# Optimization experiments

Measured on AMD Instinct MI355X. Metric: run time of the kernel, lower is better.

Reference implementation:

```python
import jax, jax.numpy as jnp
import numpy as np

D_EV, D_RGB, D_FUSED, D_REASON = 128, 128, 384, 384
D_INNER, D_STATE, D_CONV, DT_RANK = 2 * D_REASON, 16, 4, (D_REASON + 15) // 16
B, L = 4, 1024
LN_EPS = 1e-5


def setup_inputs() -> dict:
    key = jax.random.key(0)
    ks = jax.random.split(key, 16)
    s = lambda k, shp, scale=0.02: jax.random.normal(k, shp, jnp.float32) * scale
    inp = {
        "ev_tok": jax.random.normal(ks[0], (B, L, D_EV), jnp.float32),
        "rgb_tok": jax.random.normal(ks[1], (B, L, D_RGB), jnp.float32),
        "W_ev": s(ks[2], (D_EV, D_FUSED // 2)), "b_ev": jnp.zeros((D_FUSED // 2,), jnp.float32),
        "W_rgb": s(ks[3], (D_RGB, D_FUSED // 2)), "b_rgb": jnp.zeros((D_FUSED // 2,), jnp.float32),
        "ln_g": jnp.ones((D_FUSED,), jnp.float32), "ln_b": jnp.zeros((D_FUSED,), jnp.float32),
        "W_proj": s(ks[4], (D_FUSED, D_REASON)), "b_proj": jnp.zeros((D_REASON,), jnp.float32),
        "W_in": s(ks[5], (D_REASON, 2 * D_INNER)),
        "conv_w": s(ks[6], (D_INNER, 1, D_CONV), 0.1), "conv_b": jnp.zeros((D_INNER,), jnp.float32),
        "W_x": s(ks[7], (D_INNER, DT_RANK + 2 * D_STATE)),
        "W_dt": s(ks[8], (DT_RANK, D_INNER), 0.1), "b_dt": s(ks[9], (D_INNER,), 0.1),
        "A_log": jnp.tile(jnp.log(jnp.arange(1, D_STATE + 1, dtype=jnp.float32)), (D_INNER, 1)),
        "D_skip": jnp.ones((D_INNER,), jnp.float32),
        "W_out": s(ks[10], (D_INNER, D_REASON)),
    }
    return inp


def _selective_scan(u, delta, A, Bm, Cm, D_skip):
    # u, delta: [B,L,d]; Bm, Cm: [B,L,n]; A: [d,n]; D_skip: [d]
    deltaA = jnp.exp(delta[..., None] * A)                       # [B,L,d,n]
    deltaBu = delta[..., None] * Bm[:, :, None, :] * u[..., None]  # [B,L,d,n]

    def step(h, inp):
        dA, dBu, C_t = inp
        h = dA * h + dBu                                         # [B,d,n]
        y = jnp.einsum('bdn,bn->bd', h, C_t)
        return h, y

    h0 = jnp.zeros((u.shape[0], A.shape[0], A.shape[1]), u.dtype)
    xs = (jnp.moveaxis(deltaA, 1, 0), jnp.moveaxis(deltaBu, 1, 0), jnp.moveaxis(Cm, 1, 0))
    _, ys = jax.lax.scan(step, h0, xs)                           # [L,B,d]
    return jnp.moveaxis(ys, 0, 1) + u * D_skip


def _mamba_block(x, W_in, conv_w, conv_b, W_x, W_dt, b_dt, A_log, D_skip, W_out):
    xr = x @ W_in                                                # [B,L,2*d_inner]
    u, res = jnp.split(xr, 2, axis=-1)
    # causal depthwise conv over time
    uc = jnp.swapaxes(u, 1, 2)                                   # [B,d_inner,L]
    uc = jax.lax.conv_general_dilated(uc, conv_w, (1,), [(D_CONV - 1, 0)],
                                      dimension_numbers=('NCH', 'OIH', 'NCH'),
                                      feature_group_count=D_INNER)
    u = jax.nn.silu(jnp.swapaxes(uc, 1, 2) + conv_b)             # [B,L,d_inner]
    x_dbl = u @ W_x                                              # [B,L,dt_rank+2n]
    dt, Bm, Cm = jnp.split(x_dbl, [DT_RANK, DT_RANK + D_STATE], axis=-1)
    delta = jax.nn.softplus(dt @ W_dt + b_dt)                    # [B,L,d_inner]
    A = -jnp.exp(A_log)                                          # [d_inner,n]
    y = _selective_scan(u, delta, A, Bm, Cm, D_skip)
    y = y * jax.nn.silu(res)
    return y @ W_out


def reference(ev_tok, rgb_tok, W_ev, b_ev, W_rgb, b_rgb, ln_g, ln_b, W_proj, b_proj,
              W_in, conv_w, conv_b, W_x, W_dt, b_dt, A_log, D_skip, W_out):
    x = jnp.concatenate([ev_tok @ W_ev + b_ev, rgb_tok @ W_rgb + b_rgb], axis=-1)
    mu = jnp.mean(x, axis=-1, keepdims=True)
    var = jnp.mean(jnp.square(x - mu), axis=-1, keepdims=True)
    x = (x - mu) * jax.lax.rsqrt(var + LN_EPS) * ln_g + ln_b
    x = x @ W_proj + b_proj                                      # [B,L,d_reason]
    return _mamba_block(x, W_in, conv_w, conv_b, W_x, W_dt, b_dt, A_log, D_skip, W_out)
```

## Files before the change

kernel.cpp:

```cpp
#include <hip/hip_runtime.h>
#include <cstddef>
#include <cstdint>

#define L_SEQ 1024
#define NCHUNK 64
#define CLEN 16

typedef __bf16 bf16x8 __attribute__((ext_vector_type(8)));
typedef float f32x4 __attribute__((ext_vector_type(4)));

__device__ __forceinline__ float silu_f(float x) {
    return x / (1.f + __expf(-x));
}

__device__ __forceinline__ float exp2_fast(float x) {
    return exp2f(x);
}

__device__ __forceinline__ unsigned short f2bf(float x) {
    union { float f; unsigned int u; } v; v.f = x;
    unsigned int r = (v.u + 0x7fffu + ((v.u >> 16) & 1u)) >> 16;
    return (unsigned short)r;
}
__device__ __forceinline__ float bf2f(unsigned short h) {
    union { float f; unsigned int u; } v; v.u = ((unsigned int)h) << 16;
    return v.f;
}
__device__ __forceinline__ unsigned int packf(float x) {
    unsigned short h = f2bf(x);
    unsigned short l = f2bf(x - bf2f(h));
    return ((unsigned int)h << 16) | (unsigned int)l;
}
__device__ __forceinline__ float unpackf(unsigned int pk) {
    return bf2f((unsigned short)(pk >> 16)) + bf2f((unsigned short)(pk & 0xffffu));
}

template<bool APK, int EPI>
__global__ __launch_bounds__(256)
void gemm_bf3(const unsigned short* __restrict__ Ahi,
              const unsigned short* __restrict__ Alo,
              const unsigned int* __restrict__ Apk, int lda,
              const unsigned short* __restrict__ Bthi,
              const unsigned short* __restrict__ Btlo,
              const float* __restrict__ bias,
              float* __restrict__ Cf, float* __restrict__ Cf2,
              unsigned short* __restrict__ Chi, unsigned short* __restrict__ Clo,
              int ldc, int K)
{
    __shared__ unsigned short As[2][2][128][40];
    __shared__ unsigned short Bs[2][2][128][40];
    const int tid = threadIdx.x;
    const int lane = tid & 63;
    const int wave = tid >> 6;
    const int wm = wave >> 1, wn = wave & 1;

    const int gx = gridDim.x;
    const int nwg = gx * gridDim.y;
    const int lin = blockIdx.y * gx + blockIdx.x;
    const int chunk = nwg >> 3;
    const int swz = (lin & 7) * chunk + (lin >> 3);
    const int m0 = (swz / gx) * 128, n0 = (swz % gx) * 128;

    const int srow = tid >> 1, sko = (tid & 1) * 16;

    f32x4 acc[4][4];
    #pragma unroll
    for (int i = 0; i < 4; ++i)
        #pragma unroll
        for (int j = 0; j < 4; ++j) {
            f32x4 z = {0.f, 0.f, 0.f, 0.f};
            acc[i][j] = z;
        }

    const size_t aoff = (size_t)(m0 + srow) * lda + sko;
    const size_t boff = (size_t)(n0 + srow) * K + sko;

    uint4 ra[4], rb[4];

    auto load_regs = [&](int k0) {
        if constexpr (APK) {
            const unsigned int* ap = Apk + aoff + k0;
            ra[0] = *(const uint4*)(ap);
            ra[1] = *(const uint4*)(ap + 4);
            ra[2] = *(const uint4*)(ap + 8);
            ra[3] = *(const uint4*)(ap + 12);
        } else {
            ra[0] = *(const uint4*)(Ahi + aoff + k0);
            ra[1] = *(const uint4*)(Ahi + aoff + k0 + 8);
            ra[2] = *(const uint4*)(Alo + aoff + k0);
            ra[3] = *(const uint4*)(Alo + aoff + k0 + 8);
        }
        rb[0] = *(const uint4*)(Bthi + boff + k0);
        rb[1] = *(const uint4*)(Bthi + boff + k0 + 8);
        rb[2] = *(const uint4*)(Btlo + boff + k0);
        rb[3] = *(const uint4*)(Btlo + boff + k0 + 8);
    };

    auto store_lds = [&](int buf) {
        uint4 h0, h1, l0, l1;
        if constexpr (APK) {
            uint4 p0 = ra[0], p1 = ra[1], p2 = ra[2], p3 = ra[3];
            h0.x = (p0.x >> 16) | (p0.y & 0xffff0000u);
            h0.y = (p0.z >> 16) | (p0.w & 0xffff0000u);
            h0.z = (p1.x >> 16) | (p1.y & 0xffff0000u);
            h0.w = (p1.z >> 16) | (p1.w & 0xffff0000u);
            h1.x = (p2.x >> 16) | (p2.y & 0xffff0000u);
            h1.y = (p2.z >> 16) | (p2.w & 0xffff0000u);
            h1.z = (p3.x >> 16) | (p3.y & 0xffff0000u);
            h1.w = (p3.z >> 16) | (p3.w & 0xffff0000u);
            l0.x = (p0.x & 0xffffu) | (p0.y << 16);
            l0.y = (p0.z & 0xffffu) | (p0.w << 16);
            l0.z = (p1.x & 0xffffu) | (p1.y << 16);
            l0.w = (p1.z & 0xffffu) | (p1.w << 16);
            l1.x = (p2.x & 0xffffu) | (p2.y << 16);
            l1.y = (p2.z & 0xffffu) | (p2.w << 16);
            l1.z = (p3.x & 0xffffu) | (p3.y << 16);
            l1.w = (p3.z & 0xffffu) | (p3.w << 16);
        } else {
            h0 = ra[0]; h1 = ra[1]; l0 = ra[2]; l1 = ra[3];
        }
        *(uint4*)&As[buf][0][srow][sko]     = h0;
        *(uint4*)&As[buf][0][srow][sko + 8] = h1;
        *(uint4*)&As[buf][1][srow][sko]     = l0;
        *(uint4*)&As[buf][1][srow][sko + 8] = l1;
        *(uint4*)&Bs[buf][0][srow][sko]     = rb[0];
        *(uint4*)&Bs[buf][0][srow][sko + 8] = rb[1];
        *(uint4*)&Bs[buf][1][srow][sko]     = rb[2];
        *(uint4*)&Bs[buf][1][srow][sko + 8] = rb[3];
    };

    const int fr = lane & 15, kq = lane >> 4;

    load_regs(0);
    store_lds(0);
    __syncthreads();

    int cur = 0;
    for (int k0 = 32; ; k0 += 32) {
        const bool more = k0 < K;
        if (more) load_regs(k0);
        {
            bf16x8 aH[4], aL[4];
            #pragma unroll
            for (int i = 0; i < 4; ++i) {
                aH[i] = *(const bf16x8*)&As[cur][0][wm * 64 + i * 16 + fr][kq * 8];
                aL[i] = *(const bf16x8*)&As[cur][1][wm * 64 + i * 16 + fr][kq * 8];
            }
            #pragma unroll
            for (int j = 0; j < 4; ++j) {
                bf16x8 bH = *(const bf16x8*)&Bs[cur][0][wn * 64 + j * 16 + fr][kq * 8];
                bf16x8 bL = *(const bf16x8*)&Bs[cur][1][wn * 64 + j * 16 + fr][kq * 8];
                #pragma unroll
                for (int i = 0; i < 4; ++i)
                    acc[i][j] = __builtin_amdgcn_mfma_f32_16x16x32_bf16(aH[i], bH, acc[i][j], 0, 0, 0);
                #pragma unroll
                for (int i = 0; i < 4; ++i)
                    acc[i][j] = __builtin_amdgcn_mfma_f32_16x16x32_bf16(aL[i], bH, acc[i][j], 0, 0, 0);
                #pragma unroll
                for (int i = 0; i < 4; ++i)
                    acc[i][j] = __builtin_amdgcn_mfma_f32_16x16x32_bf16(aH[i], bL, acc[i][j], 0, 0, 0);
            }
        }
        if (!more) break;
        store_lds(cur ^ 1);
        __syncthreads();
        cur ^= 1;
    }

    const int col = lane & 15, rq = lane >> 4;
    #pragma unroll
    for (int j = 0; j < 4; ++j) {
        int nn = n0 + wn * 64 + j * 16 + col;
        float bv = 0.f;
        if constexpr (EPI == 0 || EPI == 1) { if (bias) bv = bias[nn]; }
        if constexpr (EPI == 2) { if (nn >= 32 && nn < 800) bv = bias[nn - 32]; }
        #pragma unroll
        for (int i = 0; i < 4; ++i) {
            int mb = m0 + wm * 64 + i * 16 + rq * 4;
            #pragma unroll
            for (int r = 0; r < 4; ++r) {
                float o = acc[i][j][r] + bv;
                if constexpr (EPI == 0) {
                    Cf[(size_t)(mb + r) * ldc + nn] = o;
                } else if constexpr (EPI == 1) {
                    unsigned short h = f2bf(o);
                    Chi[(size_t)(mb + r) * ldc + nn] = h;
                    Clo[(size_t)(mb + r) * ldc + nn] = f2bf(o - bf2f(h));
                } else {
                    if (nn < 32) {
                        Cf2[(size_t)(mb + r) * 32 + nn] = o;
                    } else if (nn < 800) {
                        float sp = fmaxf(o, 0.f) + log1pf(expf(-fabsf(o)));
                        Cf[(size_t)(mb + r) * ldc + (nn - 32)] = sp;
                    }
                }
            }
        }
    }
}

__device__ __forceinline__ void wcvt_body(const float* __restrict__ W,
                                          unsigned short* __restrict__ Thi,
                                          unsigned short* __restrict__ Tlo,
                                          int K, int N, int nx, int local, int tid,
                                          float* t )
{
    const int n0 = (local % nx) * 32, k0 = (local / nx) * 32;
    const int r = tid >> 3, c4 = (tid & 7) * 4;
    float4 v = *(const float4*)(W + (size_t)(k0 + r) * N + n0 + c4);
    t[r * 33 + c4 + 0] = v.x; t[r * 33 + c4 + 1] = v.y;
    t[r * 33 + c4 + 2] = v.z; t[r * 33 + c4 + 3] = v.w;
    __syncthreads();
    unsigned short hs[4], ls[4];
    #pragma unroll
    for (int j = 0; j < 4; ++j) {
        float x = t[(c4 + j) * 33 + r];
        hs[j] = f2bf(x);
        ls[j] = f2bf(x - bf2f(hs[j]));
    }
    size_t o = (size_t)(n0 + r) * K + k0 + c4;
    uint2 hv, lv;
    hv.x = (unsigned)hs[0] | ((unsigned)hs[1] << 16);
    hv.y = (unsigned)hs[2] | ((unsigned)hs[3] << 16);
    lv.x = (unsigned)ls[0] | ((unsigned)ls[1] << 16);
    lv.y = (unsigned)ls[2] | ((unsigned)ls[3] << 16);
    *(uint2*)(Thi + o) = hv;
    *(uint2*)(Tlo + o) = lv;
}

__global__ __launch_bounds__(256)
void prep_all(const float* __restrict__ W_proj, const float* __restrict__ W_in,
              const float* __restrict__ W_out, const float* __restrict__ W_x,
              const float* __restrict__ W_dt,
              const float* __restrict__ W_ev, const float* __restrict__ W_rgb,
              const float* __restrict__ b_ev, const float* __restrict__ b_rgb,
              const float* __restrict__ ev, const float* __restrict__ rgb,
              unsigned short* __restrict__ wtp_hi, unsigned short* __restrict__ wtp_lo,
              unsigned short* __restrict__ wti_hi, unsigned short* __restrict__ wti_lo,
              unsigned short* __restrict__ wto_hi, unsigned short* __restrict__ wto_lo,
              unsigned short* __restrict__ btc_hi, unsigned short* __restrict__ btc_lo,
              unsigned short* __restrict__ wct_hi, unsigned short* __restrict__ wct_lo,
              float* __restrict__ biascat, unsigned int* __restrict__ apk)
{
    __shared__ float t[32 * 33];
    const int blk = blockIdx.x;
    const int tid = threadIdx.x;
    if (blk < 144) {
        wcvt_body(W_proj, wtp_hi, wtp_lo, 384, 384, 12, blk, tid, t);
    } else if (blk < 720) {
        wcvt_body(W_in, wti_hi, wti_lo, 384, 1536, 48, blk - 144, tid, t);
    } else if (blk < 1008) {
        wcvt_body(W_out, wto_hi, wto_lo, 768, 384, 12, blk - 720, tid, t);
    } else if (blk < 1392) {
        const int flat = (blk - 1008) * 256 + tid;
        const int r = flat / 768, k = flat % 768;
        const int row = (r < 32) ? r : (768 + r);
        float val = (r < 32) ? W_x[(size_t)k * 56 + 24 + r] : 0.f;
        unsigned short h = f2bf(val);
        btc_hi[(size_t)row * 768 + k] = h;
        btc_lo[(size_t)row * 768 + k] = f2bf(val - bf2f(h));
    } else if (blk < 3696) {
        const int flat = (blk - 1392) * 256 + tid;
        const int j = flat / 768, k = flat % 768;
        const float* xp = W_x + (size_t)k * 56;
        float acc = 0.f;
        #pragma unroll
        for (int r = 0; r < 24; ++r)
            acc = fmaf(xp[r], W_dt[(size_t)r * 768 + j], acc);
        unsigned short h = f2bf(acc);
        btc_hi[(size_t)(32 + j) * 768 + k] = h;
        btc_lo[(size_t)(32 + j) * 768 + k] = f2bf(acc - bf2f(h));
    } else if (blk < 4082) {
        const int flat = (blk - 3696) * 256 + tid;
        if (flat < 384 * 256) {
            const int n = flat >> 8, k = flat & 255;
            float val = 0.f;
            if (n < 192) { if (k < 128) val = W_ev[(size_t)k * 192 + n]; }
            else         { if (k >= 128) val = W_rgb[(size_t)(k - 128) * 192 + (n - 192)]; }
            unsigned short h = f2bf(val);
            wct_hi[flat] = h;
            wct_lo[flat] = f2bf(val - bf2f(h));
        } else if (flat < 384 * 256 + 384) {
            const int i = flat - 384 * 256;
            biascat[i] = (i < 192) ? b_ev[i] : b_rgb[i - 192];
        }
    } else {
        const int idx = (blk - 4082) * 1024 + tid * 4;
        const int m = idx >> 8, kk = idx & 255;
        #pragma unroll
        for (int q = 0; q < 4; ++q) {
            int k = kk + q;
            float val = (k < 128) ? ev[(size_t)m * 128 + k] : rgb[(size_t)m * 128 + k - 128];
            apk[(size_t)m * 256 + k] = packf(val);
        }
    }
}

__global__ __launch_bounds__(256)
void ln2(unsigned short* __restrict__ hi, unsigned short* __restrict__ lo,
         const float* __restrict__ g, const float* __restrict__ b)
{
    const int lane = threadIdx.x & 63;
    const int row = blockIdx.x * 4 + (threadIdx.x >> 6);
    unsigned short* ph = hi + (size_t)row * 384;
    unsigned short* pl = lo + (size_t)row * 384;
    float v[6];
    #pragma unroll
    for (int i = 0; i < 6; ++i) {
        int c = i * 64 + lane;
        v[i] = bf2f(ph[c]) + bf2f(pl[c]);
    }
    float s = v[0] + v[1] + v[2] + v[3] + v[4] + v[5];
    #pragma unroll
    for (int m = 32; m >= 1; m >>= 1) s += __shfl_xor(s, m);
    const float mu = s * (1.f / 384.f);
    float q = 0.f;
    #pragma unroll
    for (int i = 0; i < 6; ++i) { float dv = v[i] - mu; q = fmaf(dv, dv, q); }
    #pragma unroll
    for (int m = 32; m >= 1; m >>= 1) q += __shfl_xor(q, m);
    const float inv = 1.f / sqrtf(q * (1.f / 384.f) + 1e-5f);
    #pragma unroll
    for (int i = 0; i < 6; ++i) {
        int c = i * 64 + lane;
        float o = (v[i] - mu) * inv * g[c] + b[c];
        unsigned short h = f2bf(o);
        ph[c] = h;
        pl[c] = f2bf(o - bf2f(h));
    }
}

__global__ __launch_bounds__(256)
void conv_pack(const float* __restrict__ xr, const float* __restrict__ conv_w,
               const float* __restrict__ conv_b, unsigned int* __restrict__ upk)
{
    const int d = blockIdx.x * 256 + threadIdx.x;
    const int t0 = blockIdx.z * L_SEQ + blockIdx.y * 16;
    const float w0 = conv_w[d * 4 + 0], w1 = conv_w[d * 4 + 1];
    const float w2 = conv_w[d * 4 + 2], w3 = conv_w[d * 4 + 3];
    const float cb = conv_b[d];
    const float* xp = xr + (size_t)t0 * 1536 + d;
    float x1, x2, x3;
    if (blockIdx.y == 0) { x1 = x2 = x3 = 0.f; }
    else {
        x1 = xp[-1 * 1536];
        x2 = xp[-2 * 1536];
        x3 = xp[-3 * 1536];
    }
    unsigned int* op = upk + (size_t)t0 * 768 + d;
    #pragma unroll 4
    for (int i = 0; i < 16; ++i) {
        float cur = xp[i * 1536];
        float a = cb;
        a = fmaf(x3, w0, a);
        a = fmaf(x2, w1, a);
        a = fmaf(x1, w2, a);
        a = fmaf(cur, w3, a);
        op[i * 768] = packf(silu_f(a));
        x3 = x2; x2 = x1; x1 = cur;
    }
}

__global__ __launch_bounds__(256)
void scan_a2(const float* __restrict__ delta, const unsigned int* __restrict__ upk,
             const float* __restrict__ bc, const float* __restrict__ A_log,
             float* __restrict__ dsum_out, float* __restrict__ Bc)
{
    __shared__ float Bsh[CLEN][16];
    const int tid = threadIdx.x;
    const int d = blockIdx.x * 256 + tid;
    const int c = blockIdx.y, b = blockIdx.z;
    const int row0 = b * L_SEQ + c * CLEN;
    {
        int t = tid >> 4, n = tid & 15;
        Bsh[t][n] = bc[(size_t)(row0 + t) * 32 + n];
    }
    float AL2[16];
    {
        const float* ap = A_log + d * 16;
        #pragma unroll
        for (int n = 0; n < 16; ++n)
            AL2[n] = -__expf(ap[n]) * 1.44269504f;
    }
    __syncthreads();
    float h[16];
    #pragma unroll
    for (int n = 0; n < 16; ++n) h[n] = 0.f;
    float dsum = 0.f;
    const float* dp = delta + (size_t)row0 * 768 + d;
    const unsigned int* up = upk + (size_t)row0 * 768 + d;
    #pragma unroll 4
    for (int t = 0; t < CLEN; ++t) {
        float dt = dp[t * 768];
        float ut = unpackf(up[t * 768]);
        float du = dt * ut;
        dsum += dt;
        #pragma unroll
        for (int n = 0; n < 16; ++n) {
            float dA = exp2_fast(dt * AL2[n]);
            h[n] = fmaf(dA, h[n], du * Bsh[t][n]);
        }
    }
    dsum_out[(size_t)(b * 768 + d) * NCHUNK + c] = dsum;
    float* bcp = Bc + (((size_t)(b * 768 + d)) * NCHUNK + c) * 16;
    #pragma unroll
    for (int n = 0; n < 16; ++n) bcp[n] = h[n];
}

__global__ __launch_bounds__(256)
void scan_b2(const float* __restrict__ dsum, const float* __restrict__ A_log,
             float* __restrict__ BcHin)
{
    const size_t flat = (size_t)blockIdx.x * 256 + threadIdx.x;
    const size_t bd = flat >> 4;
    const int n = (int)(flat & 15);
    const int d = (int)(bd % 768);
    const float AL2 = -__expf(A_log[d * 16 + n]) * 1.44269504f;
    const float* dsp = dsum + bd * NCHUNK;
    const size_t base = bd * (NCHUNK * 16) + n;
    float h = 0.f;
    for (int c = 0; c < NCHUNK; ++c) {
        size_t i = base + (size_t)c * 16;
        float a = exp2_fast(AL2 * dsp[c]);
        float bb = BcHin[i];
        BcHin[i] = h;
        h = fmaf(a, h, bb);
    }
}

__global__ __launch_bounds__(256)
void scan_c2(float* __restrict__ delta, const unsigned int* __restrict__ upk,
             const float* __restrict__ bc, const float* __restrict__ A_log,
             const float* __restrict__ Hin, const float* __restrict__ D_skip,
             const float* __restrict__ xr)
{
    __shared__ float Bsh[CLEN][16];
    __shared__ float Csh[CLEN][16];
    const int tid = threadIdx.x;
    const int d = blockIdx.x * 256 + tid;
    const int c = blockIdx.y, b = blockIdx.z;
    const int row0 = b * L_SEQ + c * CLEN;
    {
        int t = tid >> 4, n = tid & 15;
        const float* xp = bc + (size_t)(row0 + t) * 32;
        Bsh[t][n] = xp[n];
        Csh[t][n] = xp[16 + n];
    }
    float AL2[16];
    {
        const float* ap = A_log + d * 16;
        #pragma unroll
        for (int n = 0; n < 16; ++n)
            AL2[n] = -__expf(ap[n]) * 1.44269504f;
    }
    float h[16];
    {
        const float* hp = Hin + (((size_t)(b * 768 + d)) * NCHUNK + c) * 16;
        #pragma unroll
        for (int n = 0; n < 16; ++n) h[n] = hp[n];
    }
    const float Ds = D_skip[d];
    __syncthreads();
    float* dp = delta + (size_t)row0 * 768 + d;
    const unsigned int* up = upk + (size_t)row0 * 768 + d;
    const float* rp = xr + (size_t)row0 * 1536 + 768 + d;
    #pragma unroll 4
    for (int t = 0; t < CLEN; ++t) {
        float dt = dp[t * 768];
        float ut = unpackf(up[t * 768]);
        float du = dt * ut;
        float y = 0.f;
        #pragma unroll
        for (int n = 0; n < 16; ++n) {
            float dA = exp2_fast(dt * AL2[n]);
            h[n] = fmaf(dA, h[n], du * Bsh[t][n]);
            y = fmaf(h[n], Csh[t][n], y);
        }
        float res = rp[t * 1536];
        float gy = fmaf(ut, Ds, y) * silu_f(res);
        dp[t * 768] = __builtin_bit_cast(float, packf(gy));
    }
}

extern "C" void kernel_launch(void* const* d_in, const int* in_sizes, int n_in,
                              void* d_out, int out_size, void* d_ws, size_t ws_size,
                              hipStream_t stream)
{
    const float* ev     = (const float*)d_in[0];
    const float* rgb    = (const float*)d_in[1];
    const float* W_ev   = (const float*)d_in[2];
    const float* b_ev   = (const float*)d_in[3];
    const float* W_rgb  = (const float*)d_in[4];
    const float* b_rgb  = (const float*)d_in[5];
    const float* ln_g   = (const float*)d_in[6];
    const float* ln_b   = (const float*)d_in[7];
    const float* W_proj = (const float*)d_in[8];
    const float* b_proj = (const float*)d_in[9];
    const float* W_in   = (const float*)d_in[10];
    const float* conv_w = (const float*)d_in[11];
    const float* conv_b = (const float*)d_in[12];
    const float* W_x    = (const float*)d_in[13];
    const float* W_dt   = (const float*)d_in[14];
    const float* b_dt   = (const float*)d_in[15];
    const float* A_log  = (const float*)d_in[16];
    const float* D_skip = (const float*)d_in[17];
    const float* W_out  = (const float*)d_in[18];
    float* out = (float*)d_out;

    float* ws = (float*)d_ws;
    unsigned short* xfh  = (unsigned short*)ws;
    unsigned short* xfl  = xfh + 1572864;
    float* dsum          = ws;
    float* bc            = ws + 196608;
    unsigned short* xmmh = (unsigned short*)(ws + 1572864);
    unsigned short* xmml = xmmh + 1572864;
    unsigned int* upk    = (unsigned int*)(ws + 1572864);
    float* xr            = ws + 4718592;
    unsigned int* apk    = (unsigned int*)xr;
    float* delta         = ws + 11239424;
    float* BcHin         = ws + 14385152;
    unsigned short* wtp_hi = (unsigned short*)BcHin;
    unsigned short* wtp_lo = wtp_hi + 147456;
    unsigned short* wti_hi = wtp_lo + 147456;
    unsigned short* wti_lo = wti_hi + 589824;
    unsigned short* btc_hi = (unsigned short*)(BcHin + 737280);
    unsigned short* btc_lo = btc_hi + 688128;
    unsigned short* wct_hi = (unsigned short*)(BcHin + 1425408);
    unsigned short* wct_lo = wct_hi + 98304;
    float* biascat         = BcHin + 1523712;
    unsigned short* wto_hi = (unsigned short*)(ws + 17530880);
    unsigned short* wto_lo = wto_hi + 294912;

    dim3 blk(256);

    prep_all<<<5106, blk, 0, stream>>>(
        W_proj, W_in, W_out, W_x, W_dt, W_ev, W_rgb, b_ev, b_rgb, ev, rgb,
        wtp_hi, wtp_lo, wti_hi, wti_lo, wto_hi, wto_lo,
        btc_hi, btc_lo, wct_hi, wct_lo, biascat, apk);

    gemm_bf3<true, 1><<<dim3(3, 32), blk, 0, stream>>>(
        nullptr, nullptr, apk, 256, wct_hi, wct_lo, biascat,
        nullptr, nullptr, xfh, xfl, 384, 256);
    ln2<<<1024, blk, 0, stream>>>(xfh, xfl, ln_g, ln_b);
    gemm_bf3<false, 1><<<dim3(3, 32), blk, 0, stream>>>(
        xfh, xfl, nullptr, 384, wtp_hi, wtp_lo, b_proj,
        nullptr, nullptr, xmmh, xmml, 384, 384);
    gemm_bf3<false, 0><<<dim3(12, 32), blk, 0, stream>>>(
        xmmh, xmml, nullptr, 384, wti_hi, wti_lo, nullptr,
        xr, nullptr, nullptr, nullptr, 1536, 384);
    conv_pack<<<dim3(3, 64, 4), blk, 0, stream>>>(xr, conv_w, conv_b, upk);
    gemm_bf3<true, 2><<<dim3(7, 32), blk, 0, stream>>>(
        nullptr, nullptr, upk, 768, btc_hi, btc_lo, b_dt,
        delta, bc, nullptr, nullptr, 768, 768);
    scan_a2<<<dim3(3, NCHUNK, 4), blk, 0, stream>>>(delta, upk, bc, A_log, dsum, BcHin);
    scan_b2<<<192, blk, 0, stream>>>(dsum, A_log, BcHin);
    scan_c2<<<dim3(3, NCHUNK, 4), blk, 0, stream>>>(delta, upk, bc, A_log, BcHin, D_skip, xr);
    gemm_bf3<true, 0><<<dim3(3, 32), blk, 0, stream>>>(
        nullptr, nullptr, (const unsigned int*)delta, 768, wto_hi, wto_lo, nullptr,
        out, nullptr, nullptr, nullptr, 384, 768);
}
```

Before: 282.7 us.

## Fold W_proj into W_in, add split-K GEMMs with combine kernels

Precomputes W_proj·W_in, and b_proj·W_in as a bias, inside prep, so the projection GEMM disappears from the activation path and the in-projection reads the LayerNorm output directly. The fusion GEMM, the x_proj/dt GEMM and the output GEMM gain split-K over blockIdx.z so that small grids fill more compute units. Partial sums are reduced in new combine kernels, and softplus plus bias move into the combine step. This trades more launches and extra partial-buffer traffic for higher occupancy, and rounding changes slightly because a precomputed weight product is used.

```diff
diff --git a/kernel.cpp b/kernel.cpp
--- a/kernel.cpp
+++ b/kernel.cpp
@@ -12,10 +12,7 @@
 __device__ __forceinline__ float silu_f(float x) {
     return x / (1.f + __expf(-x));
 }
-
-__device__ __forceinline__ float exp2_fast(float x) {
-    return exp2f(x);
-}
+__device__ __forceinline__ float exp2_fast(float x) { return exp2f(x); }
 
 __device__ __forceinline__ unsigned short f2bf(float x) {
     union { float f; unsigned int u; } v; v.f = x;
@@ -35,7 +32,7 @@
     return bf2f((unsigned short)(pk >> 16)) + bf2f((unsigned short)(pk & 0xffffu));
 }
 
-template<bool APK, int EPI>
+template<bool APK, int EPI, int SPLITS>
 __global__ __launch_bounds__(256)
 void gemm_bf3(const unsigned short* __restrict__ Ahi,
               const unsigned short* __restrict__ Alo,
@@ -45,7 +42,7 @@
               const float* __restrict__ bias,
               float* __restrict__ Cf, float* __restrict__ Cf2,
               unsigned short* __restrict__ Chi, unsigned short* __restrict__ Clo,
-              int ldc, int K)
+              int Ks, int Ktot, int Nw)
 {
     __shared__ unsigned short As[2][2][128][40];
     __shared__ unsigned short Bs[2][2][128][40];
@@ -57,9 +54,10 @@
     const int gx = gridDim.x;
     const int nwg = gx * gridDim.y;
     const int lin = blockIdx.y * gx + blockIdx.x;
-    const int chunk = nwg >> 3;
-    const int swz = (lin & 7) * chunk + (lin >> 3);
+    const int swz = ((nwg & 7) == 0) ? ((lin & 7) * (nwg >> 3) + (lin >> 3)) : lin;
     const int m0 = (swz / gx) * 128, n0 = (swz % gx) * 128;
+    const int z = (SPLITS > 1) ? blockIdx.z : 0;
+    const int kbeg = z * Ks;
 
     const int srow = tid >> 1, sko = (tid & 1) * 16;
 
@@ -68,12 +66,12 @@
     for (int i = 0; i < 4; ++i)
         #pragma unroll
         for (int j = 0; j < 4; ++j) {
-            f32x4 z = {0.f, 0.f, 0.f, 0.f};
-            acc[i][j] = z;
+            f32x4 zz = {0.f, 0.f, 0.f, 0.f};
+            acc[i][j] = zz;
         }
 
     const size_t aoff = (size_t)(m0 + srow) * lda + sko;
-    const size_t boff = (size_t)(n0 + srow) * K + sko;
+    const size_t boff = (size_t)(n0 + srow) * Ktot + sko;
 
     uint4 ra[4], rb[4];
 
@@ -131,13 +129,14 @@
 
     const int fr = lane & 15, kq = lane >> 4;
 
-    load_regs(0);
+    load_regs(kbeg);
     store_lds(0);
     __syncthreads();
 
     int cur = 0;
-    for (int k0 = 32; ; k0 += 32) {
-        const bool more = k0 < K;
+    const int kend = kbeg + Ks;
+    for (int k0 = kbeg + 32; ; k0 += 32) {
+        const bool more = k0 < kend;
         if (more) load_regs(k0);
         {
             bf16x8 aH[4], aL[4];
@@ -167,32 +166,33 @@
         cur ^= 1;
     }
 
+    float* myP = nullptr;
+    if constexpr (EPI == 3) {
+        float* base = (2 * z >= SPLITS) ? Cf2 : Cf;
+        int sub = z - ((2 * z >= SPLITS) ? SPLITS / 2 : 0);
+        myP = base + (size_t)sub * (size_t)(gridDim.y * 128) * Nw;
+    }
     const int col = lane & 15, rq = lane >> 4;
     #pragma unroll
     for (int j = 0; j < 4; ++j) {
         int nn = n0 + wn * 64 + j * 16 + col;
         float bv = 0.f;
-        if constexpr (EPI == 0 || EPI == 1) { if (bias) bv = bias[nn]; }
-        if constexpr (EPI == 2) { if (nn >= 32 && nn < 800) bv = bias[nn - 32]; }
+        if constexpr (EPI == 1 || EPI == 4) { if (bias) bv = bias[nn]; }
         #pragma unroll
         for (int i = 0; i < 4; ++i) {
             int mb = m0 + wm * 64 + i * 16 + rq * 4;
             #pragma unroll
             for (int r = 0; r < 4; ++r) {
                 float o = acc[i][j][r] + bv;
-                if constexpr (EPI == 0) {
-                    Cf[(size_t)(mb + r) * ldc + nn] = o;
-                } else if constexpr (EPI == 1) {
+                if constexpr (EPI == 1) {
                     unsigned short h = f2bf(o);
-                    Chi[(size_t)(mb + r) * ldc + nn] = h;
-                    Clo[(size_t)(mb + r) * ldc + nn] = f2bf(o - bf2f(h));
-                } else {
-                    if (nn < 32) {
-                        Cf2[(size_t)(mb + r) * 32 + nn] = o;
-                    } else if (nn < 800) {
-                        float sp = fmaxf(o, 0.f) + log1pf(expf(-fabsf(o)));
-                        Cf[(size_t)(mb + r) * ldc + (nn - 32)] = sp;
-                    }
+                    Chi[(size_t)(mb + r) * Nw + nn] = h;
+                    Clo[(size_t)(mb + r) * Nw + nn] = f2bf(o - bf2f(h));
+                } else if constexpr (EPI == 3) {
+                    if (nn < Nw) myP[(size_t)(mb + r) * Nw + nn] = o;
+                } else if constexpr (EPI == 4) {
+                    if (nn < 768) Cf[(size_t)(mb + r) * 768 + nn] = o;
+                    else          Cf2[(size_t)(mb + r) * 768 + (nn - 768)] = o;
                 }
             }
         }
@@ -231,7 +231,7 @@
 __global__ __launch_bounds__(256)
 void prep_all(const float* __restrict__ W_proj, const float* __restrict__ W_in,
               const float* __restrict__ W_out, const float* __restrict__ W_x,
-              const float* __restrict__ W_dt,
+              const float* __restrict__ W_dt, const float* __restrict__ b_proj,
               const float* __restrict__ W_ev, const float* __restrict__ W_rgb,
               const float* __restrict__ b_ev, const float* __restrict__ b_rgb,
               const float* __restrict__ ev, const float* __restrict__ rgb,
@@ -240,7 +240,9 @@
               unsigned short* __restrict__ wto_hi, unsigned short* __restrict__ wto_lo,
               unsigned short* __restrict__ btc_hi, unsigned short* __restrict__ btc_lo,
               unsigned short* __restrict__ wct_hi, unsigned short* __restrict__ wct_lo,
-              float* __restrict__ biascat, unsigned int* __restrict__ apk)
+              unsigned short* __restrict__ wpd_hi, unsigned short* __restrict__ wpd_lo,
+              float* __restrict__ biascat, float* __restrict__ bias_pi,
+              unsigned int* __restrict__ apk)
 {
     __shared__ float t[32 * 33];
     const int blk = blockIdx.x;
@@ -284,7 +286,7 @@
             const int i = flat - 384 * 256;
             biascat[i] = (i < 192) ? b_ev[i] : b_rgb[i - 192];
         }
-    } else {
+    } else if (blk < 5106) {
         const int idx = (blk - 4082) * 1024 + tid * 4;
         const int m = idx >> 8, kk = idx & 255;
         #pragma unroll
@@ -293,22 +295,38 @@
             float val = (k < 128) ? ev[(size_t)m * 128 + k] : rgb[(size_t)m * 128 + k - 128];
             apk[(size_t)m * 256 + k] = packf(val);
         }
-    }
-}
-
-__global__ __launch_bounds__(256)
-void ln2(unsigned short* __restrict__ hi, unsigned short* __restrict__ lo,
-         const float* __restrict__ g, const float* __restrict__ b)
+    } else if (blk < 5682) {
+        const int flat = (blk - 5106) * 256 + tid;
+        float val = W_proj[flat];
+        unsigned short h = f2bf(val);
+        wpd_hi[flat] = h;
+        wpd_lo[flat] = f2bf(val - bf2f(h));
+    } else {
+        const int j = (blk - 5682) * 256 + tid;
+        float acc = 0.f;
+        for (int i = 0; i < 384; ++i)
+            acc = fmaf(b_proj[i], W_in[(size_t)i * 1536 + j], acc);
+        bias_pi[j] = acc;
+    }
+}
+
+__global__ __launch_bounds__(256)
+void ln2(const float* __restrict__ ep0, const float* __restrict__ ep1,
+         const float* __restrict__ biascat,
+         const float* __restrict__ g, const float* __restrict__ b,
+         unsigned short* __restrict__ hi, unsigned short* __restrict__ lo)
 {
     const int lane = threadIdx.x & 63;
     const int row = blockIdx.x * 4 + (threadIdx.x >> 6);
+    const float* p0 = ep0 + (size_t)row * 384;
+    const float* p1 = ep1 + (size_t)row * 384;
     unsigned short* ph = hi + (size_t)row * 384;
     unsigned short* pl = lo + (size_t)row * 384;
     float v[6];
     #pragma unroll
     for (int i = 0; i < 6; ++i) {
         int c = i * 64 + lane;
-        v[i] = bf2f(ph[c]) + bf2f(pl[c]);
+        v[i] = p0[c] + p1[c] + biascat[c];
     }
     float s = v[0] + v[1] + v[2] + v[3] + v[4] + v[5];
     #pragma unroll
@@ -331,7 +349,7 @@
 }
 
 __global__ __launch_bounds__(256)
-void conv_pack(const float* __restrict__ xr, const float* __restrict__ conv_w,
+void conv_pack(const float* __restrict__ u_pre, const float* __restrict__ conv_w,
                const float* __restrict__ conv_b, unsigned int* __restrict__ upk)
 {
     const int d = blockIdx.x * 256 + threadIdx.x;
@@ -339,18 +357,18 @@
     const float w0 = conv_w[d * 4 + 0], w1 = conv_w[d * 4 + 1];
     const float w2 = conv_w[d * 4 + 2], w3 = conv_w[d * 4 + 3];
     const float cb = conv_b[d];
-    const float* xp = xr + (size_t)t0 * 1536 + d;
+    const float* xp = u_pre + (size_t)t0 * 768 + d;
     float x1, x2, x3;
     if (blockIdx.y == 0) { x1 = x2 = x3 = 0.f; }
     else {
-        x1 = xp[-1 * 1536];
-        x2 = xp[-2 * 1536];
-        x3 = xp[-3 * 1536];
+        x1 = xp[-1 * 768];
+        x2 = xp[-2 * 768];
+        x3 = xp[-3 * 768];
     }
     unsigned int* op = upk + (size_t)t0 * 768 + d;
     #pragma unroll 4
     for (int i = 0; i < 16; ++i) {
-        float cur = xp[i * 1536];
+        float cur = xp[i * 768];
         float a = cb;
         a = fmaf(x3, w0, a);
         a = fmaf(x2, w1, a);
@@ -359,6 +377,48 @@
         op[i * 768] = packf(silu_f(a));
         x3 = x2; x2 = x1; x1 = cur;
     }
+}
+
+__global__ __launch_bounds__(256)
+void combine_fused(const float* __restrict__ P0, const float* __restrict__ P1,
+                   const float* __restrict__ b_dt,
+                   float* __restrict__ bc, float* __restrict__ delta)
+{
+    const int g = blockIdx.x * 256 + threadIdx.x;
+    const int m = g / 200, c0 = (g % 200) * 4;
+    const float* a = P0 + (size_t)m * 800 + c0;
+    const float* bb = P1 + (size_t)m * 800 + c0;
+    float4 s0 = *(const float4*)a;
+    float4 s1 = *(const float4*)bb;
+    float sv[4] = {s0.x + s1.x, s0.y + s1.y, s0.z + s1.z, s0.w + s1.w};
+    #pragma unroll
+    for (int j = 0; j < 4; ++j) {
+        int col = c0 + j;
+        if (col < 32) {
+            bc[(size_t)m * 32 + col] = sv[j];
+        } else {
+            float o = sv[j] + b_dt[col - 32];
+            delta[(size_t)m * 768 + col - 32] = fmaxf(o, 0.f) + log1pf(expf(-fabsf(o)));
+        }
+    }
+}
+
+__global__ __launch_bounds__(256)
+void combine_out(const float* __restrict__ PA, const float* __restrict__ PB,
+                 float* __restrict__ out)
+{
+    const int g = blockIdx.x * 256 + threadIdx.x;
+    const size_t o = (size_t)g * 4;
+    float4 a0 = *(const float4*)(PA + o);
+    float4 a1 = *(const float4*)(PA + 1572864 + o);
+    float4 a2 = *(const float4*)(PB + o);
+    float4 a3 = *(const float4*)(PB + 1572864 + o);
+    float4 r;
+    r.x = a0.x + a1.x + a2.x + a3.x;
+    r.y = a0.y + a1.y + a2.y + a3.y;
+    r.z = a0.z + a1.z + a2.z + a3.z;
+    r.w = a0.w + a1.w + a2.w + a3.w;
+    *(float4*)(out + o) = r;
 }
 
 __global__ __launch_bounds__(256)
@@ -432,7 +492,7 @@
 void scan_c2(float* __restrict__ delta, const unsigned int* __restrict__ upk,
              const float* __restrict__ bc, const float* __restrict__ A_log,
              const float* __restrict__ Hin, const float* __restrict__ D_skip,
-             const float* __restrict__ xr)
+             const float* __restrict__ res)
 {
     __shared__ float Bsh[CLEN][16];
     __shared__ float Csh[CLEN][16];
@@ -463,7 +523,7 @@
     __syncthreads();
     float* dp = delta + (size_t)row0 * 768 + d;
     const unsigned int* up = upk + (size_t)row0 * 768 + d;
-    const float* rp = xr + (size_t)row0 * 1536 + 768 + d;
+    const float* rp = res + (size_t)row0 * 768 + d;
     #pragma unroll 4
     for (int t = 0; t < CLEN; ++t) {
         float dt = dp[t * 768];
@@ -476,8 +536,8 @@
             h[n] = fmaf(dA, h[n], du * Bsh[t][n]);
             y = fmaf(h[n], Csh[t][n], y);
         }
-        float res = rp[t * 1536];
-        float gy = fmaf(ut, Ds, y) * silu_f(res);
+        float rr = rp[t * 768];
+        float gy = fmaf(ut, Ds, y) * silu_f(rr);
         dp[t * 768] = __builtin_bit_cast(float, packf(gy));
     }
 }
@@ -508,54 +568,73 @@
     float* out = (float*)d_out;
 
     float* ws = (float*)d_ws;
-    unsigned short* xfh  = (unsigned short*)ws;
-    unsigned short* xfl  = xfh + 1572864;
-    float* dsum          = ws;
-    float* bc            = ws + 196608;
-    unsigned short* xmmh = (unsigned short*)(ws + 1572864);
-    unsigned short* xmml = xmmh + 1572864;
-    unsigned int* upk    = (unsigned int*)(ws + 1572864);
-    float* xr            = ws + 4718592;
-    unsigned int* apk    = (unsigned int*)xr;
-    float* delta         = ws + 11239424;
-    float* BcHin         = ws + 14385152;
-    unsigned short* wtp_hi = (unsigned short*)BcHin;
+    const size_t O0 = 0;
+    const size_t O1 = 3145728;
+    const size_t O2 = 6422528;
+    const size_t O3 = 9568256;
+    const size_t O4 = 12713984;
+    const size_t O5 = 16056320;
+
+    float* res   = ws + O0;
+    unsigned int* apk = (unsigned int*)(ws + O0);
+    float* u_pre = ws + O1;
+    float* ep0   = ws + O1;
+    float* ep1   = ws + O1 + 1572864;
+    float* P0    = ws + O1;
+    float* outPA = ws + O1;
+    unsigned int* upk = (unsigned int*)(ws + O2);
+    unsigned short* xfh = (unsigned short*)(ws + O2);
+    unsigned short* xfl = xfh + 1572864;
+    unsigned short* wpi_hi = (unsigned short*)(ws + O2 + 1572864);
+    unsigned short* wpi_lo = wpi_hi + 589824;
+    float* delta = ws + O3;
+    unsigned short* wtp_hi = (unsigned short*)(ws + O3);
     unsigned short* wtp_lo = wtp_hi + 147456;
-    unsigned short* wti_hi = wtp_lo + 147456;
+    unsigned short* wpd_hi = wtp_lo + 147456;
+    unsigned short* wpd_lo = wpd_hi + 147456;
+    unsigned short* wti_hi = wpd_lo + 147456;
     unsigned short* wti_lo = wti_hi + 589824;
-    unsigned short* btc_hi = (unsigned short*)(BcHin + 737280);
+    unsigned short* btc_hi = (unsigned short*)(ws + O3 + 884736);
     unsigned short* btc_lo = btc_hi + 688128;
-    unsigned short* wct_hi = (unsigned short*)(BcHin + 1425408);
+    float* P1    = ws + O4;
+    float* dsum  = ws + O4;
+    float* BcHin = ws + O4 + 196608;
+    float* outPB = ws + O4;
+    unsigned short* wct_hi = (unsigned short*)(ws + O5);
     unsigned short* wct_lo = wct_hi + 98304;
-    float* biascat         = BcHin + 1523712;
-    unsigned short* wto_hi = (unsigned short*)(ws + 17530880);
-    unsigned short* wto_lo = wto_hi + 294912;
+    float* biascat = ws + O5 + 98304;
+    float* bias_pi = ws + O5 + 98688;
+    unsigned short* wto_hi = (unsigned short*)(ws + O5 + 100224);
+    unsigned short* wto_lo = wto_hi + 589824;
+    float* bc    = ws + O5 + 690048;
 
     dim3 blk(256);
 
-    prep_all<<<5106, blk, 0, stream>>>(
-        W_proj, W_in, W_out, W_x, W_dt, W_ev, W_rgb, b_ev, b_rgb, ev, rgb,
+    prep_all<<<5688, blk, 0, stream>>>(
+        W_proj, W_in, W_out, W_x, W_dt, b_proj, W_ev, W_rgb, b_ev, b_rgb, ev, rgb,
         wtp_hi, wtp_lo, wti_hi, wti_lo, wto_hi, wto_lo,
-        btc_hi, btc_lo, wct_hi, wct_lo, biascat, apk);
-
-    gemm_bf3<true, 1><<<dim3(3, 32), blk, 0, stream>>>(
-        nullptr, nullptr, apk, 256, wct_hi, wct_lo, biascat,
-        nullptr, nullptr, xfh, xfl, 384, 256);
-    ln2<<<1024, blk, 0, stream>>>(xfh, xfl, ln_g, ln_b);
-    gemm_bf3<false, 1><<<dim3(3, 32), blk, 0, stream>>>(
-        xfh, xfl, nullptr, 384, wtp_hi, wtp_lo, b_proj,
-        nullptr, nullptr, xmmh, xmml, 384, 384);
-    gemm_bf3<false, 0><<<dim3(12, 32), blk, 0, stream>>>(
-        xmmh, xmml, nullptr, 384, wti_hi, wti_lo, nullptr,
-        xr, nullptr, nullptr, nullptr, 1536, 384);
-    conv_pack<<<dim3(3, 64, 4), blk, 0, stream>>>(xr, conv_w, conv_b, upk);
-    gemm_bf3<true, 2><<<dim3(7, 32), blk, 0, stream>>>(
-        nullptr, nullptr, upk, 768, btc_hi, btc_lo, b_dt,
-        delta, bc, nullptr, nullptr, 768, 768);
+        btc_hi, btc_lo, wct_hi, wct_lo, wpd_hi, wpd_lo, biascat, bias_pi, apk);
+
+    gemm_bf3<true, 3, 2><<<dim3(3, 32, 2), blk, 0, stream>>>(
+        nullptr, nullptr, apk, 256, wct_hi, wct_lo, nullptr,
+        ep0, ep1, nullptr, nullptr, 128, 256, 384);
+    gemm_bf3<false, 1, 1><<<dim3(3, 12), blk, 0, stream>>>(
+        wti_hi, wti_lo, nullptr, 384, wpd_hi, wpd_lo, nullptr,
+        nullptr, nullptr, wpi_hi, wpi_lo, 384, 384, 384);
+    ln2<<<1024, blk, 0, stream>>>(ep0, ep1, biascat, ln_g, ln_b, xfh, xfl);
+    gemm_bf3<false, 4, 1><<<dim3(12, 32), blk, 0, stream>>>(
+        xfh, xfl, nullptr, 384, wpi_hi, wpi_lo, bias_pi,
+        u_pre, res, nullptr, nullptr, 384, 384, 1536);
+    conv_pack<<<dim3(3, 64, 4), blk, 0, stream>>>(u_pre, conv_w, conv_b, upk);
+    gemm_bf3<true, 3, 2><<<dim3(7, 32, 2), blk, 0, stream>>>(
+        nullptr, nullptr, upk, 768, btc_hi, btc_lo, nullptr,
+        P0, P1, nullptr, nullptr, 384, 768, 800);
+    combine_fused<<<3200, blk, 0, stream>>>(P0, P1, b_dt, bc, delta);
     scan_a2<<<dim3(3, NCHUNK, 4), blk, 0, stream>>>(delta, upk, bc, A_log, dsum, BcHin);
     scan_b2<<<192, blk, 0, stream>>>(dsum, A_log, BcHin);
-    scan_c2<<<dim3(3, NCHUNK, 4), blk, 0, stream>>>(delta, upk, bc, A_log, BcHin, D_skip, xr);
-    gemm_bf3<true, 0><<<dim3(3, 32), blk, 0, stream>>>(
+    scan_c2<<<dim3(3, NCHUNK, 4), blk, 0, stream>>>(delta, upk, bc, A_log, BcHin, D_skip, res);
+    gemm_bf3<true, 3, 4><<<dim3(3, 32, 4), blk, 0, stream>>>(
         nullptr, nullptr, (const unsigned int*)delta, 768, wto_hi, wto_lo, nullptr,
-        out, nullptr, nullptr, nullptr, 384, 768);
-}
+        outPA, outPB, nullptr, nullptr, 192, 768, 384);
+    combine_out<<<1536, blk, 0, stream>>>(outPA, outPB, out);
+}
```

Result: faster. 266.0 us (-5.9%).
